# Performance work log

Measured on AMD Instinct MI355X. Metric: run time of the kernel, lower is better.

## Reference

```python
import jax, jax.numpy as jnp
import numpy as np

N_NODES = 100000
N_EDGES = 3200000
N_GRAPHS = 256
NEG_SLOPE = 0.2  # PyG GATConv default


def setup_inputs() -> dict:
    key = jax.random.key(0)
    ks = jax.random.split(key, 20)
    x = jax.random.normal(ks[0], (N_NODES, 20), jnp.float32)
    edge_index = jax.random.randint(ks[1], (2, N_EDGES), 0, N_NODES, dtype=jnp.int32)
    batch = jnp.sort(jax.random.randint(ks[2], (N_NODES,), 0, N_GRAPHS, dtype=jnp.int32))
    s = 0.1
    return {
        "x": x,
        "edge_index": edge_index,
        "batch": batch,
        "num_graphs": N_GRAPHS,
        "w_gat": jax.random.normal(ks[3], (20, 4, 16), jnp.float32) * s,
        "att_src": jax.random.normal(ks[4], (4, 16), jnp.float32) * s,
        "att_dst": jax.random.normal(ks[5], (4, 16), jnp.float32) * s,
        "b_gat": jax.random.normal(ks[6], (64,), jnp.float32) * s,
        "w_fuse": jax.random.normal(ks[7], (64, 64), jnp.float32) * s,
        "b_fuse": jax.random.normal(ks[8], (64,), jnp.float32) * s,
        "w_h1": jax.random.normal(ks[9], (64, 32), jnp.float32) * s,
        "b_h1": jax.random.normal(ks[10], (32,), jnp.float32) * s,
        "w_h2": jax.random.normal(ks[11], (32, 16), jnp.float32) * s,
        "b_h2": jax.random.normal(ks[12], (16,), jnp.float32) * s,
        "w_h3": jax.random.normal(ks[13], (16, 16), jnp.float32) * s,
        "b_h3": jax.random.normal(ks[14], (16,), jnp.float32) * s,
        "w_ev": jax.random.normal(ks[15], (16, 3), jnp.float32) * s,
        "b_ev": jax.random.normal(ks[16], (3,), jnp.float32) * s,
        "w_env": jax.random.normal(ks[17], (16, 3), jnp.float32) * s,
        "b_env": jax.random.normal(ks[18], (3,), jnp.float32) * s,
    }


def gat_conv(x, edge_index, w_gat, att_src, att_dst, b_gat, num_nodes):
    # Linear projection per head: [N, H, C]
    xh = jnp.einsum('nf,fhc->nhc', x, w_gat)
    # add self loops (PyG add_self_loops=True)
    loop = jnp.arange(num_nodes, dtype=edge_index.dtype)
    src = jnp.concatenate([edge_index[0], loop])  # source j
    dst = jnp.concatenate([edge_index[1], loop])  # target i
    # per-node attention terms [N, H]
    a_s = jnp.einsum('nhc,hc->nh', xh, att_src)
    a_d = jnp.einsum('nhc,hc->nh', xh, att_dst)
    # per-edge logit, leaky relu
    logit = jax.nn.leaky_relu(a_s[src] + a_d[dst], NEG_SLOPE)  # [E, H]
    # segment softmax over destination node
    m = jax.ops.segment_max(logit, dst, num_segments=num_nodes)
    e = jnp.exp(logit - m[dst])
    z = jax.ops.segment_sum(e, dst, num_segments=num_nodes)
    alpha = e / z[dst]  # [E, H]
    # weighted scatter-aggregate of source features
    msg = xh[src] * alpha[:, :, None]  # [E, H, C]
    out = jax.ops.segment_sum(msg, dst, num_segments=num_nodes)  # [N, H, C]
    return out.reshape(num_nodes, -1) + b_gat  # concat heads + bias


def reference(x, edge_index, batch, num_graphs, w_gat, att_src, att_dst, b_gat,
              w_fuse, b_fuse, w_h1, b_h1, w_h2, b_h2, w_h3, b_h3,
              w_ev, b_ev, w_env, b_env):
    n = x.shape[0]
    h = gat_conv(x, edge_index, w_gat, att_src, att_dst, b_gat, n)
    h = jax.nn.relu(h @ w_fuse + b_fuse)
    h = jax.nn.relu(h @ w_h1 + b_h1)
    h = jax.nn.relu(h @ w_h2 + b_h2)
    h = jax.nn.relu(h @ w_h3 + b_h3)
    # global mean pool over graphs
    sums = jax.ops.segment_sum(h, batch, num_segments=num_graphs)
    cnts = jax.ops.segment_sum(jnp.ones((n, 1), h.dtype), batch, num_segments=num_graphs)
    g = sums / jnp.maximum(cnts, 1.0)
    out_event = g @ w_ev + b_ev
    out_env = g @ w_env + b_env
    return (out_event, out_env)
```

## Files before the change

kernel.cpp:

```cpp
#include <hip/hip_runtime.h>
#include <hip/hip_bf16.h>
#include <hip/hip_fp16.h>

#define FIN 20
#define HEADS 4
#define F 64
#define NEG_SLOPE 0.2f
#define AP 68
#define BSHIFT 8
#define BMASK 255
#define NVX 8
#define BCAPX 1408
#define MAXBUCK 512
#define BIN_EPT 16

__global__ void __launch_bounds__(256)
prep_bin(const float* __restrict__ x,
         const float* __restrict__ w_gat,
         const float* __restrict__ att_src,
         const float* __restrict__ att_dst,
         __half* __restrict__ xh,
         float* __restrict__ a_s,
         float* __restrict__ a_d,
         const int* __restrict__ ei, int E, int nbuck,
         int* __restrict__ gcount, int* __restrict__ bucketData,
         int n_nodes, int nbP)
{
    if (blockIdx.x < nbP) {
        __shared__ __align__(16) float w[FIN * F];
        __shared__ float asrc[F];
        __shared__ float adst[F];
        for (int i = threadIdx.x; i < FIN * F; i += 256) w[i] = w_gat[i];
        if (threadIdx.x < F) {
            asrc[threadIdx.x] = att_src[threadIdx.x];
            adst[threadIdx.x] = att_dst[threadIdx.x];
        }
        __syncthreads();

        int n = blockIdx.x * 256 + threadIdx.x;
        if (n >= n_nodes) return;

        float xv[FIN];
#pragma unroll
        for (int q = 0; q < FIN / 4; ++q) {
            float4 x4 = *(const float4*)&x[(size_t)n * FIN + q * 4];
            xv[q * 4 + 0] = x4.x; xv[q * 4 + 1] = x4.y;
            xv[q * 4 + 2] = x4.z; xv[q * 4 + 3] = x4.w;
        }

        float as[HEADS] = {0.f, 0.f, 0.f, 0.f};
        float ad[HEADS] = {0.f, 0.f, 0.f, 0.f};

#pragma unroll
        for (int j4 = 0; j4 < F / 4; ++j4) {
            float4 acc = make_float4(0.f, 0.f, 0.f, 0.f);
#pragma unroll
            for (int k = 0; k < FIN; ++k) {
                float4 w4 = *(const float4*)&w[k * F + j4 * 4];
                acc.x += xv[k] * w4.x;
                acc.y += xv[k] * w4.y;
                acc.z += xv[k] * w4.z;
                acc.w += xv[k] * w4.w;
            }
            __half2 p0 = __floats2half2_rn(acc.x, acc.y);
            __half2 p1 = __floats2half2_rn(acc.z, acc.w);
            float2 st;
            ((__half2*)&st)[0] = p0;
            ((__half2*)&st)[1] = p1;
            *(float2*)&xh[(size_t)n * F + j4 * 4] = st;

            int h = j4 >> 2;
            int jb = j4 * 4;
            as[h] += acc.x * asrc[jb] + acc.y * asrc[jb + 1] + acc.z * asrc[jb + 2] + acc.w * asrc[jb + 3];
            ad[h] += acc.x * adst[jb] + acc.y * adst[jb + 1] + acc.z * adst[jb + 2] + acc.w * adst[jb + 3];
        }
#pragma unroll
        for (int h = 0; h < HEADS; ++h) {
            a_s[(size_t)n * HEADS + h] = as[h];
            a_d[(size_t)n * HEADS + h] = ad[h];
        }
    } else {
        __shared__ int lcnt[MAXBUCK];
        __shared__ int lbase[MAXBUCK];
        for (int i = threadIdx.x; i < nbuck; i += 256) lcnt[i] = 0;
        __syncthreads();

        const int bb = blockIdx.x - nbP;
        const int vx = bb & (NVX - 1);
        int* __restrict__ gc = gcount + vx * nbuck;
        int* __restrict__ bdat = bucketData + (size_t)vx * nbuck * BCAPX;

        int base = bb * (256 * BIN_EPT);
        int b_[BIN_EPT], w_[BIN_EPT], r_[BIN_EPT];
#pragma unroll
        for (int j = 0; j < BIN_EPT; ++j) {
            int e = base + j * 256 + threadIdx.x;
            if (e < E) {
                int src = ei[e];
                int dst = ei[E + e];
                b_[j] = dst >> BSHIFT;
                w_[j] = ((dst & BMASK) << 17) | src;
                r_[j] = atomicAdd(&lcnt[b_[j]], 1);
            } else b_[j] = -1;
        }
        __syncthreads();
        for (int i = threadIdx.x; i < nbuck; i += 256) {
            int c = lcnt[i];
            lbase[i] = c ? atomicAdd(&gc[i], c) : 0;
        }
        __syncthreads();
#pragma unroll
        for (int j = 0; j < BIN_EPT; ++j) {
            if (b_[j] >= 0) {
                int p = lbase[b_[j]] + r_[j];
                if (p < BCAPX) bdat[(size_t)b_[j] * BCAPX + p] = w_[j];
            }
        }
    }
}

__global__ void __launch_bounds__(1024)
csr_build(const int* __restrict__ bucketData, const int* __restrict__ gcount,
          int* __restrict__ off, int* __restrict__ srcs,
          int n_nodes, int total_edges, int nbuck)
{
    __shared__ int hist[256];
    __shared__ int psum[256];
    int b = blockIdx.x;
    int t = threadIdx.x;
    int node0 = b << BSHIFT;
    int nnode = n_nodes - node0; if (nnode > 256) nnode = 256;

    if (t < 256) {
        int acc = 0;
        for (int i = t; i < b; i += 256) {
            int s = 0;
#pragma unroll
            for (int seg = 0; seg < NVX; ++seg) {
                int c = gcount[seg * nbuck + i];
                s += c < BCAPX ? c : BCAPX;
            }
            acc += s;
        }
        psum[t] = acc;
    }
    __syncthreads();
    for (int d = 128; d > 0; d >>= 1) {
        if (t < d) psum[t] += psum[t + d];
        __syncthreads();
    }
    int base = psum[0] + node0;
    __syncthreads();
    if (b == 0 && t == 0) off[n_nodes] = total_edges;

    if (t < 256) hist[t] = 0;
    __syncthreads();

    int cS[NVX];
    int wv[NVX * 2];
    int rk[NVX * 2];
#pragma unroll
    for (int seg = 0; seg < NVX; ++seg) {
        int cntS = gcount[seg * nbuck + b]; cS[seg] = cntS < BCAPX ? cntS : BCAPX;
        const int* bd = bucketData + ((size_t)seg * nbuck + b) * BCAPX;
        {
            bool v = t < cS[seg];
            int w = v ? bd[t] : 0;
            wv[seg * 2] = w;
            rk[seg * 2] = v ? atomicAdd(&hist[w >> 17], 1) : 0;
        }
        {
            bool v = (t + 1024) < cS[seg];
            int w = v ? bd[t + 1024] : 0;
            wv[seg * 2 + 1] = w;
            rk[seg * 2 + 1] = v ? atomicAdd(&hist[w >> 17], 1) : 0;
        }
    }
    __syncthreads();

    if (t < 256) psum[t] = (t < nnode) ? hist[t] + 1 : 0;
    __syncthreads();
    for (int d = 1; d < 256; d <<= 1) {
        int w = (t >= d && t < 256) ? psum[t - d] : 0;
        __syncthreads();
        if (t < 256) psum[t] += w;
        __syncthreads();
    }
    int ex = (t == 0 || t >= 256) ? 0 : psum[t - 1];
    __syncthreads();
    if (t < nnode) {
        int o = base + ex;
        off[node0 + t] = o;
        srcs[o] = node0 + t;
        hist[t] = o + 1;
    }
    __syncthreads();

#pragma unroll
    for (int seg = 0; seg < NVX; ++seg) {
        if (t < cS[seg]) {
            int w = wv[seg * 2];
            srcs[hist[w >> 17] + rk[seg * 2]] = w & 0x1FFFF;
        }
        if ((t + 1024) < cS[seg]) {
            int w = wv[seg * 2 + 1];
            srcs[hist[w >> 17] + rk[seg * 2 + 1]] = w & 0x1FFFF;
        }
    }
}

__global__ void __launch_bounds__(256, 4)
gat_mlp(const int* __restrict__ off,
        const int* __restrict__ srcs,
        const float* __restrict__ a_s,
        const float* __restrict__ a_d,
        const __half* __restrict__ xh,
        const int* __restrict__ batch,
        const float* __restrict__ b_gat,
        const float* __restrict__ w_fuse, const float* __restrict__ b_fuse,
        const float* __restrict__ w_h1, const float* __restrict__ b_h1,
        const float* __restrict__ w_h2, const float* __restrict__ b_h2,
        const float* __restrict__ w_h3, const float* __restrict__ b_h3,
        float* __restrict__ gsum,
        int n_nodes)
{
    __shared__ __align__(16) __half wfh[64 * 64];
    __shared__ __align__(16) __half w1h[64 * 32];
    __shared__ __align__(16) float w2[32 * 16];
    __shared__ __align__(16) float w3[16 * 16];
    __shared__ __align__(16) float bf[64];
    __shared__ __align__(16) float b1[32], b2[16], b3[16];
    __shared__ int gids[32];
    __shared__ __align__(16) float act[32 * AP];

    for (int i = threadIdx.x; i < 64 * 64; i += 256) wfh[i] = __float2half(w_fuse[i]);
    for (int i = threadIdx.x; i < 64 * 32; i += 256) w1h[i] = __float2half(w_h1[i]);
    for (int i = threadIdx.x; i < 32 * 16; i += 256) w2[i] = w_h2[i];
    for (int i = threadIdx.x; i < 16 * 16; i += 256) w3[i] = w_h3[i];
    if (threadIdx.x < 64) bf[threadIdx.x] = b_fuse[threadIdx.x];
    else if (threadIdx.x < 96)  b1[threadIdx.x - 64] = b_h1[threadIdx.x - 64];
    else if (threadIdx.x < 112) b2[threadIdx.x - 96] = b_h2[threadIdx.x - 96];
    else if (threadIdx.x < 128) b3[threadIdx.x - 112] = b_h3[threadIdx.x - 112];
    else if (threadIdx.x >= 224) {
        int nn = blockIdx.x * 32 + (threadIdx.x - 224);
        gids[threadIdx.x - 224] = (nn < n_nodes) ? batch[nn] : -1;
    }

    {
        const int node_l2 = threadIdx.x >> 3;
        const int part = threadIdx.x & 7;
        const int n = blockIdx.x * 32 + node_l2;
        const int h = part >> 1;
        const int g8 = (threadIdx.x & 63) >> 3;

        float acc[8] = {0.f, 0.f, 0.f, 0.f, 0.f, 0.f, 0.f, 0.f};
        float zacc = 0.f;
        bool active = (n < n_nodes);
        if (active) {
            int kb = off[n];
            int ke = off[n + 1];
            float adh = a_d[n * 4 + h];

            int i0 = kb + part;          i0 = i0 < ke - 1 ? i0 : ke - 1;
            int sA = srcs[i0];
            int i1 = kb + 8 + part;      i1 = i1 < ke - 1 ? i1 : ke - 1;
            int sNxt = srcs[i1];

            int sj[8];
#pragma unroll
            for (int j = 0; j < 8; ++j) sj[j] = __shfl(sA, g8 * 8 + j, 64);
            float4 rawA[8]; float aslA[8];
#pragma unroll
            for (int j = 0; j < 8; ++j) {
                rawA[j] = *(const float4*)&xh[(size_t)sj[j] * F + part * 8];
                aslA[j] = a_s[sj[j] * 4 + h];
            }

            float4 rawB[8]; float aslB[8];
            int base = kb;
            while (true) {
                bool hasB = (base + 8 < ke);
                if (hasB) {
#pragma unroll
                    for (int j = 0; j < 8; ++j) sj[j] = __shfl(sNxt, g8 * 8 + j, 64);
#pragma unroll
                    for (int j = 0; j < 8; ++j) {
                        rawB[j] = *(const float4*)&xh[(size_t)sj[j] * F + part * 8];
                        aslB[j] = a_s[sj[j] * 4 + h];
                    }
                    int i2 = base + 16 + part;  i2 = i2 < ke - 1 ? i2 : ke - 1;
                    sNxt = srcs[i2];
                }
#pragma unroll
                for (int j = 0; j < 8; ++j) {
                    float l = aslA[j] + adh;
                    l = l > 0.f ? l : NEG_SLOPE * l;
                    float e = (base + j < ke) ? __expf(l) : 0.f;
                    zacc += e;
                    const __half2* hp = (const __half2*)&rawA[j];
                    float2 c0 = __half22float2(hp[0]);
                    float2 c1 = __half22float2(hp[1]);
                    float2 c2 = __half22float2(hp[2]);
                    float2 c3 = __half22float2(hp[3]);
                    acc[0] += e * c0.x; acc[1] += e * c0.y;
                    acc[2] += e * c1.x; acc[3] += e * c1.y;
                    acc[4] += e * c2.x; acc[5] += e * c2.y;
                    acc[6] += e * c3.x; acc[7] += e * c3.y;
                }
                base += 8;
                if (!hasB) break;

                bool hasC = (base + 8 < ke);
                if (hasC) {
#pragma unroll
                    for (int j = 0; j < 8; ++j) sj[j] = __shfl(sNxt, g8 * 8 + j, 64);
#pragma unroll
                    for (int j = 0; j < 8; ++j) {
                        rawA[j] = *(const float4*)&xh[(size_t)sj[j] * F + part * 8];
                        aslA[j] = a_s[sj[j] * 4 + h];
                    }
                    int i2 = base + 16 + part;  i2 = i2 < ke - 1 ? i2 : ke - 1;
                    sNxt = srcs[i2];
                }
#pragma unroll
                for (int j = 0; j < 8; ++j) {
                    float l = aslB[j] + adh;
                    l = l > 0.f ? l : NEG_SLOPE * l;
                    float e = (base + j < ke) ? __expf(l) : 0.f;
                    zacc += e;
                    const __half2* hp = (const __half2*)&rawB[j];
                    float2 c0 = __half22float2(hp[0]);
                    float2 c1 = __half22float2(hp[1]);
                    float2 c2 = __half22float2(hp[2]);
                    float2 c3 = __half22float2(hp[3]);
                    acc[0] += e * c0.x; acc[1] += e * c0.y;
                    acc[2] += e * c1.x; acc[3] += e * c1.y;
                    acc[4] += e * c2.x; acc[5] += e * c2.y;
                    acc[6] += e * c3.x; acc[7] += e * c3.y;
                }
                base += 8;
                if (!hasC) break;
            }
        }
        float inv = active ? (1.f / zacc) : 0.f;
        float4 bg0 = *(const float4*)&b_gat[part * 8];
        float4 bg1 = *(const float4*)&b_gat[part * 8 + 4];
        float4 o0, o1;
        o0.x = acc[0] * inv + bg0.x; o0.y = acc[1] * inv + bg0.y;
        o0.z = acc[2] * inv + bg0.z; o0.w = acc[3] * inv + bg0.w;
        o1.x = acc[4] * inv + bg1.x; o1.y = acc[5] * inv + bg1.y;
        o1.z = acc[6] * inv + bg1.z; o1.w = acc[7] * inv + bg1.w;
        *(float4*)&act[node_l2 * AP + part * 8]     = o0;
        *(float4*)&act[node_l2 * AP + part * 8 + 4] = o1;
    }
    __syncthreads();

    const int node_l = threadIdx.x >> 4;
    const int part   = threadIdx.x & 15;

    float* rowA = &act[node_l * AP];
    float* rowB = &act[(node_l + 16) * AP];

    {
        float4 aA = *(const float4*)&bf[part * 4];
        float4 aB = aA;
#pragma unroll
        for (int k4 = 0; k4 < 16; ++k4) {
            float4 hA = *(const float4*)&rowA[k4 * 4];
            float4 hB = *(const float4*)&rowB[k4 * 4];
#pragma unroll
            for (int q = 0; q < 4; ++q) {
                const __half2* wp = (const __half2*)&wfh[(k4 * 4 + q) * 64 + part * 4];
                float2 wlo = __half22float2(wp[0]);
                float2 whi = __half22float2(wp[1]);
                float hva = (q == 0) ? hA.x : (q == 1) ? hA.y : (q == 2) ? hA.z : hA.w;
                float hvb = (q == 0) ? hB.x : (q == 1) ? hB.y : (q == 2) ? hB.z : hB.w;
                aA.x += hva * wlo.x; aA.y += hva * wlo.y;
                aA.z += hva * whi.x; aA.w += hva * whi.y;
                aB.x += hvb * wlo.x; aB.y += hvb * wlo.y;
                aB.z += hvb * whi.x; aB.w += hvb * whi.y;
            }
        }
        aA.x = aA.x > 0.f ? aA.x : 0.f; aA.y = aA.y > 0.f ? aA.y : 0.f;
        aA.z = aA.z > 0.f ? aA.z : 0.f; aA.w = aA.w > 0.f ? aA.w : 0.f;
        aB.x = aB.x > 0.f ? aB.x : 0.f; aB.y = aB.y > 0.f ? aB.y : 0.f;
        aB.z = aB.z > 0.f ? aB.z : 0.f; aB.w = aB.w > 0.f ? aB.w : 0.f;
        *(float4*)&rowA[part * 4] = aA;
        *(float4*)&rowB[part * 4] = aB;
    }

    {
        float axA = b1[part * 2], ayA = b1[part * 2 + 1];
        float axB = axA, ayB = ayA;
#pragma unroll
        for (int k4 = 0; k4 < 16; ++k4) {
            float4 hA = *(const float4*)&rowA[k4 * 4];
            float4 hB = *(const float4*)&rowB[k4 * 4];
#pragma unroll
            for (int q = 0; q < 4; ++q) {
                float2 w2f = __half22float2(*(const __half2*)&w1h[(k4 * 4 + q) * 32 + part * 2]);
                float hva = (q == 0) ? hA.x : (q == 1) ? hA.y : (q == 2) ? hA.z : hA.w;
                float hvb = (q == 0) ? hB.x : (q == 1) ? hB.y : (q == 2) ? hB.z : hB.w;
                axA += hva * w2f.x; ayA += hva * w2f.y;
                axB += hvb * w2f.x; ayB += hvb * w2f.y;
            }
        }
        axA = axA > 0.f ? axA : 0.f; ayA = ayA > 0.f ? ayA : 0.f;
        axB = axB > 0.f ? axB : 0.f; ayB = ayB > 0.f ? ayB : 0.f;
        float2 uA; uA.x = axA; uA.y = ayA;
        float2 uB; uB.x = axB; uB.y = ayB;
        *(float2*)&rowA[part * 2] = uA;
        *(float2*)&rowB[part * 2] = uB;
    }

    {
        float aA = b2[part], aB = aA;
#pragma unroll
        for (int k4 = 0; k4 < 8; ++k4) {
            float4 hA = *(const float4*)&rowA[k4 * 4];
            float4 hB = *(const float4*)&rowB[k4 * 4];
            float w0 = w2[(k4 * 4 + 0) * 16 + part];
            float wq1 = w2[(k4 * 4 + 1) * 16 + part];
            float wq2 = w2[(k4 * 4 + 2) * 16 + part];
            float wq3 = w2[(k4 * 4 + 3) * 16 + part];
            aA += hA.x * w0 + hA.y * wq1 + hA.z * wq2 + hA.w * wq3;
            aB += hB.x * w0 + hB.y * wq1 + hB.z * wq2 + hB.w * wq3;
        }
        aA = aA > 0.f ? aA : 0.f;
        aB = aB > 0.f ? aB : 0.f;
        rowA[part] = aA;
        rowB[part] = aB;
    }

    {
        float aA = b3[part], aB = aA;
#pragma unroll
        for (int k4 = 0; k4 < 4; ++k4) {
            float4 hA = *(const float4*)&rowA[k4 * 4];
            float4 hB = *(const float4*)&rowB[k4 * 4];
            float w0 = w3[(k4 * 4 + 0) * 16 + part];
            float wq1 = w3[(k4 * 4 + 1) * 16 + part];
            float wq2 = w3[(k4 * 4 + 2) * 16 + part];
            float wq3 = w3[(k4 * 4 + 3) * 16 + part];
            aA += hA.x * w0 + hA.y * wq1 + hA.z * wq2 + hA.w * wq3;
            aB += hB.x * w0 + hB.y * wq1 + hB.z * wq2 + hB.w * wq3;
        }
        rowA[part] = aA > 0.f ? aA : 0.f;
        rowB[part] = aB > 0.f ? aB : 0.f;
    }
    __syncthreads();

    int g0 = gids[0], g31 = gids[31];
    if (g0 == g31 && g0 >= 0) {
        const int c = threadIdx.x & 15;
        const int r = threadIdx.x >> 4;
        w3[r * 16 + c] = act[r * AP + c] + act[(r + 16) * AP + c];
        __syncthreads();
        if (threadIdx.x < 128) w3[r * 16 + c] += w3[(r + 8) * 16 + c];
        __syncthreads();
        if (threadIdx.x < 64)  w3[r * 16 + c] += w3[(r + 4) * 16 + c];
        __syncthreads();
        if (threadIdx.x < 32)  w3[r * 16 + c] += w3[(r + 2) * 16 + c];
        __syncthreads();
        if (threadIdx.x < 16)
            atomicAdd(&gsum[g0 * 16 + threadIdx.x],
                      w3[threadIdx.x] + w3[16 + threadIdx.x]);
    } else {
        if (threadIdx.x < 16) {
            int c = threadIdx.x;
            float accg = 0.f; int cur = -2;
#pragma unroll 4
            for (int r = 0; r < 32; ++r) {
                int gid = gids[r];
                if (gid != cur) {
                    if (cur >= 0) atomicAdd(&gsum[cur * 16 + c], accg);
                    accg = 0.f; cur = gid;
                }
                if (gid >= 0) accg += act[r * AP + c];
            }
            if (cur >= 0) atomicAdd(&gsum[cur * 16 + c], accg);
        }
    }
}

__global__ void __launch_bounds__(64)
head(const float* __restrict__ gsum, const int* __restrict__ batch,
     const float* __restrict__ w_ev, const float* __restrict__ b_ev,
     const float* __restrict__ w_env, const float* __restrict__ b_env,
     float* __restrict__ out, int n_nodes, int n_graphs)
{
    __shared__ int s_bounds[2];
    __shared__ float gvec[16];

    int g = blockIdx.x;
    if (threadIdx.x < 2) {
        int target = g + threadIdx.x;
        int lo = 0, hi = n_nodes;
        while (lo < hi) { int m = (lo + hi) >> 1; if (batch[m] < target) lo = m + 1; else hi = m; }
        s_bounds[threadIdx.x] = lo;
    }
    __syncthreads();
    if (threadIdx.x < 16) {
        float cnt = (float)(s_bounds[1] - s_bounds[0]);
        cnt = cnt > 1.f ? cnt : 1.f;
        gvec[threadIdx.x] = gsum[g * 16 + threadIdx.x] / cnt;
    }
    __syncthreads();

    if (threadIdx.x < 3) {
        int j = threadIdx.x;
        float a = b_ev[j];
#pragma unroll
        for (int k = 0; k < 16; ++k) a += gvec[k] * w_ev[k * 3 + j];
        out[(size_t)g * 3 + j] = a;
    } else if (threadIdx.x < 6) {
        int j = threadIdx.x - 3;
        float a = b_env[j];
#pragma unroll
        for (int k = 0; k < 16; ++k) a += gvec[k] * w_env[k * 3 + j];
        out[(size_t)n_graphs * 3 + (size_t)g * 3 + j] = a;
    }
}

extern "C" void kernel_launch(void* const* d_in, const int* in_sizes, int n_in,
                              void* d_out, int out_size, void* d_ws, size_t ws_size,
                              hipStream_t stream)
{
    const float* x       = (const float*)d_in[0];
    const int*   ei      = (const int*)d_in[1];
    const int*   batch   = (const int*)d_in[2];
    const float* w_gat   = (const float*)d_in[4];
    const float* att_src = (const float*)d_in[5];
    const float* att_dst = (const float*)d_in[6];
    const float* b_gat   = (const float*)d_in[7];
    const float* w_fuse  = (const float*)d_in[8];
    const float* b_fuse  = (const float*)d_in[9];
    const float* w_h1    = (const float*)d_in[10];
    const float* b_h1    = (const float*)d_in[11];
    const float* w_h2    = (const float*)d_in[12];
    const float* b_h2    = (const float*)d_in[13];
    const float* w_h3    = (const float*)d_in[14];
    const float* b_h3    = (const float*)d_in[15];
    const float* w_ev    = (const float*)d_in[16];
    const float* b_ev    = (const float*)d_in[17];
    const float* w_env   = (const float*)d_in[18];
    const float* b_env   = (const float*)d_in[19];

    const int n_nodes  = in_sizes[0] / FIN;
    const int E        = in_sizes[1] / 2;
    const int n_graphs = 256;
    const int total    = E + n_nodes;
    const int nbuck    = (n_nodes + BMASK) >> BSHIFT;

    float* ws     = (float*)d_ws;
    __half* xh    = (__half*)ws;
    float* a_s    = ws   + (size_t)n_nodes * 32;
    float* a_d    = a_s  + (size_t)n_nodes * HEADS;
    int*   off    = (int*)(a_d + (size_t)n_nodes * HEADS);
    int*   srcs   = off    + n_nodes + 1;
    float* gsum   = (float*)(srcs + total);
    int*   gcount = (int*)(gsum + n_graphs * 16);
    int*   bucketData = gcount + NVX * nbuck;

    hipMemsetAsync(gsum, 0,
                   ((size_t)n_graphs * 16 + (size_t)NVX * nbuck) * sizeof(int),
                   stream);

    const int nbP = (n_nodes + 255) / 256;
    const int nbB = (E + 256 * BIN_EPT - 1) / (256 * BIN_EPT);

    prep_bin<<<nbP + nbB, 256, 0, stream>>>(
        x, w_gat, att_src, att_dst, xh, a_s, a_d,
        ei, E, nbuck, gcount, bucketData, n_nodes, nbP);

    csr_build<<<nbuck, 1024, 0, stream>>>(
        bucketData, gcount, off, srcs, n_nodes, total, nbuck);

    gat_mlp<<<(n_nodes + 31) / 32, 256, 0, stream>>>(
        off, srcs, a_s, a_d, xh, batch, b_gat,
        w_fuse, b_fuse, w_h1, b_h1, w_h2, b_h2, w_h3, b_h3,
        gsum, n_nodes);

    head<<<n_graphs, 64, 0, stream>>>(
        gsum, batch, w_ev, b_ev, w_env, b_env, (float*)d_out, n_nodes, n_graphs);
}
```

Baseline: 254.3 us.

## Stage binned edges and CSR sources in shared memory for coalesced writes

The binning blocks now prefix-sum their per-bucket counts and first gather edges into a contiguous shared-memory array. The global bucket writes then run as consecutive per-bucket runs, with a binary search recovering each item's bucket. The CSR build likewise scatters sources into a shared stage buffer and copies it out linearly, replacing random global scatters with coalesced stores. This costs more shared memory and extra barriers in the scan, which may lower occupancy. Rows with more than STCAP entries would be truncated.

Measured after the change: 242.1 us, median of 2. 1.05x faster.

```diff
diff --git a/kernel.cpp b/kernel.cpp
--- a/kernel.cpp
+++ b/kernel.cpp
@@ -13,6 +13,7 @@
 #define BCAPX 1408
 #define MAXBUCK 512
 #define BIN_EPT 16
+#define STCAP 9728
 
 __global__ void __launch_bounds__(256)
 prep_bin(const float* __restrict__ x,
@@ -82,7 +83,10 @@
     } else {
         __shared__ int lcnt[MAXBUCK];
         __shared__ int lbase[MAXBUCK];
-        for (int i = threadIdx.x; i < nbuck; i += 256) lcnt[i] = 0;
+        __shared__ int lofs[MAXBUCK];
+        __shared__ int stage2[256 * BIN_EPT];
+        const int t = threadIdx.x;
+        for (int i = t; i < MAXBUCK; i += 256) lcnt[i] = 0;
         __syncthreads();
 
         const int bb = blockIdx.x - nbP;
@@ -94,7 +98,7 @@
         int b_[BIN_EPT], w_[BIN_EPT], r_[BIN_EPT];
 #pragma unroll
         for (int j = 0; j < BIN_EPT; ++j) {
-            int e = base + j * 256 + threadIdx.x;
+            int e = base + j * 256 + t;
             if (e < E) {
                 int src = ei[e];
                 int dst = ei[E + e];
@@ -104,17 +108,50 @@
             } else b_[j] = -1;
         }
         __syncthreads();
-        for (int i = threadIdx.x; i < nbuck; i += 256) {
+
+        lofs[t] = lcnt[t];
+        lofs[256 + t] = lcnt[256 + t];
+        __syncthreads();
+        for (int d = 1; d < 256; d <<= 1) {
+            int v = (t >= d) ? lofs[t - d] : 0;
+            __syncthreads();
+            lofs[t] += v;
+            __syncthreads();
+        }
+        for (int d = 1; d < 256; d <<= 1) {
+            int v = (t >= d) ? lofs[256 + t - d] : 0;
+            __syncthreads();
+            lofs[256 + t] += v;
+            __syncthreads();
+        }
+        {
+            int tot0 = lofs[255];
+            __syncthreads();
+            lofs[256 + t] += tot0;
+            __syncthreads();
+        }
+
+#pragma unroll
+        for (int j = 0; j < BIN_EPT; ++j) {
+            if (b_[j] >= 0) {
+                int eo = b_[j] ? lofs[b_[j] - 1] : 0;
+                stage2[eo + r_[j]] = w_[j];
+            }
+        }
+        for (int i = t; i < nbuck; i += 256) {
             int c = lcnt[i];
             lbase[i] = c ? atomicAdd(&gc[i], c) : 0;
         }
         __syncthreads();
-#pragma unroll
-        for (int j = 0; j < BIN_EPT; ++j) {
-            if (b_[j] >= 0) {
-                int p = lbase[b_[j]] + r_[j];
-                if (p < BCAPX) bdat[(size_t)b_[j] * BCAPX + p] = w_[j];
-            }
+
+        int vtot = lofs[MAXBUCK - 1];
+        for (int i = t; i < vtot; i += 256) {
+            int wd = stage2[i];
+            int lo = 0, hi = nbuck;
+            while (lo < hi) { int m = (lo + hi) >> 1; if (lofs[m] < i + 1) lo = m + 1; else hi = m; }
+            int eo = lo ? lofs[lo - 1] : 0;
+            int p = lbase[lo] + (i - eo);
+            if (p < BCAPX) bdat[(size_t)lo * BCAPX + p] = wd;
         }
     }
 }
@@ -126,6 +163,8 @@
 {
     __shared__ int hist[256];
     __shared__ int psum[256];
+    __shared__ int s_w;
+    __shared__ int stage[STCAP];
     int b = blockIdx.x;
     int t = threadIdx.x;
     int node0 = b << BSHIFT;
@@ -189,24 +228,30 @@
     int ex = (t == 0 || t >= 256) ? 0 : psum[t - 1];
     __syncthreads();
     if (t < nnode) {
-        int o = base + ex;
-        off[node0 + t] = o;
-        srcs[o] = node0 + t;
-        hist[t] = o + 1;
-    }
+        off[node0 + t] = base + ex;
+        if (ex < STCAP) stage[ex] = node0 + t;
+        hist[t] = ex + 1;
+    }
+    if (t == nnode - 1) s_w = psum[t];
     __syncthreads();
 
 #pragma unroll
     for (int seg = 0; seg < NVX; ++seg) {
         if (t < cS[seg]) {
             int w = wv[seg * 2];
-            srcs[hist[w >> 17] + rk[seg * 2]] = w & 0x1FFFF;
+            int idx = hist[w >> 17] + rk[seg * 2];
+            if (idx < STCAP) stage[idx] = w & 0x1FFFF;
         }
         if ((t + 1024) < cS[seg]) {
             int w = wv[seg * 2 + 1];
-            srcs[hist[w >> 17] + rk[seg * 2 + 1]] = w & 0x1FFFF;
-        }
-    }
+            int idx = hist[w >> 17] + rk[seg * 2 + 1];
+            if (idx < STCAP) stage[idx] = w & 0x1FFFF;
+        }
+    }
+    __syncthreads();
+
+    int wcap = s_w < STCAP ? s_w : STCAP;
+    for (int i = t; i < wcap; i += 1024) srcs[base + i] = stage[i];
 }
 
 __global__ void __launch_bounds__(256, 4)
```
